# Optimization experiments

Measured on AMD Instinct MI355X. Metric: run time of the kernel, lower is better.

## Reference

```python
import jax, jax.numpy as jnp
import numpy as np
from jax import lax

LIN_DIMS = [(3200, 2048), (2048, 1024), (1024, 512), (512, 256), (256, 128),
            (128, 64), (64, 32), (32, 16), (16, 8), (8, 4), (4, 2), (2, 1)]
BN_EPS = 1e-5


def _conv(x, w, b):
    y = lax.conv_general_dilated(x, w, window_strides=(3, 3),
                                 padding=((1, 1), (1, 1)),
                                 dimension_numbers=('NCHW', 'OIHW', 'NCHW'))
    return y + b.reshape(1, -1, 1, 1)


def _bn(x, g, b):
    # training-mode BatchNorm2d: biased batch statistics over (N, H, W)
    m = jnp.mean(x, axis=(0, 2, 3), keepdims=True)
    v = jnp.var(x, axis=(0, 2, 3), keepdims=True)
    return (x - m) * lax.rsqrt(v + BN_EPS) * g.reshape(1, -1, 1, 1) + b.reshape(1, -1, 1, 1)


def setup_inputs() -> dict:
    key = jax.random.key(0)
    ks = iter(jax.random.split(key, 64))
    d = {}
    d['x'] = jax.random.normal(next(ks), (64, 512, 40, 40), jnp.float32)
    d['conv1_w'] = jax.random.normal(next(ks), (256, 512, 3, 3), jnp.float32) / np.sqrt(512 * 9)
    d['conv1_b'] = jnp.zeros((256,), jnp.float32)
    d['bn1_g'] = jnp.ones((256,), jnp.float32)
    d['bn1_b'] = jnp.zeros((256,), jnp.float32)
    d['conv2_w'] = jax.random.normal(next(ks), (128, 256, 3, 3), jnp.float32) / np.sqrt(256 * 9)
    d['conv2_b'] = jnp.zeros((128,), jnp.float32)
    d['bn2_g'] = jnp.ones((128,), jnp.float32)
    d['bn2_b'] = jnp.zeros((128,), jnp.float32)
    for i, (fin, fout) in enumerate(LIN_DIMS):
        d[f'w{i+3}'] = jax.random.normal(next(ks), (fout, fin), jnp.float32) / np.sqrt(fin)
        d[f'b{i+3}'] = jax.random.normal(next(ks), (fout,), jnp.float32) * 0.01
    return d


def reference(x, conv1_w, conv1_b, bn1_g, bn1_b, conv2_w, conv2_b, bn2_g, bn2_b,
              w3, b3, w4, b4, w5, b5, w6, b6, w7, b7, w8, b8, w9, b9,
              w10, b10, w11, b11, w12, b12, w13, b13, w14, b14):
    h = _bn(_conv(x, conv1_w, conv1_b), bn1_g, bn1_b)          # [B,256,14,14]
    h = _bn(_conv(h, conv2_w, conv2_b), bn2_g, bn2_b)          # [B,128,5,5]
    h = h.reshape(h.shape[0], 3200)
    for w, b in [(w3, b3), (w4, b4), (w5, b5), (w6, b6), (w7, b7), (w8, b8),
                 (w9, b9), (w10, b10), (w11, b11), (w12, b12), (w13, b13), (w14, b14)]:
        h = h @ w.T + b
    return jax.nn.sigmoid(h)                                   # [B,1]
```

## Files before the change

kernel.cpp:

```cpp
#include <hip/hip_runtime.h>
#include <cstdint>
#include <cstddef>

typedef short bf16x8 __attribute__((ext_vector_type(8)));
typedef float f32x4 __attribute__((ext_vector_type(4)));

__device__ __forceinline__ unsigned short f2bf(float f) {
  union { float f; unsigned u; } v; v.f = f;
  unsigned r = v.u + 0x7fffu + ((v.u >> 16) & 1u);
  return (unsigned short)(r >> 16);
}

#define GLOAD_LDS16(gp, lp)                                            \
  __builtin_amdgcn_global_load_lds(                                    \
      (const __attribute__((address_space(1))) void*)(const void*)(gp),\
      (__attribute__((address_space(3))) void*)(void*)(lp), 16, 0, 0)

__global__ __launch_bounds__(256) void cast1(const float* __restrict__ w1,
                                             unsigned short* __restrict__ W1b) {
  int i = blockIdx.x * 256 + threadIdx.x;
  float4 v = ((const float4*)w1)[i];
  ushort4 o;
  o.x = f2bf(v.x); o.y = f2bf(v.y); o.z = f2bf(v.z); o.w = f2bf(v.w);
  ((ushort4*)W1b)[i] = o;
}

__global__ __launch_bounds__(256) void im2col1(const float* __restrict__ x,
                                               unsigned short* __restrict__ A1) {
  __shared__ float buf[64 * 126];
  int t = threadIdx.x;
  int cc = blockIdx.x, oh = blockIdx.y, n = blockIdx.z;
  int ci0 = cc * 64;
  int ih0 = oh * 3 - 1;
  for (int rowid = t; rowid < 192; rowid += 256) {
    int c = rowid / 3, r = rowid - c * 3;
    buf[c * 126 + r * 42 + 0] = 0.f;
    buf[c * 126 + r * 42 + 41] = 0.f;
  }
  for (int idx = t; idx < 1920; idx += 256) {
    int row = idx / 10, ch = idx - row * 10;
    int c = row / 3, r = row - c * 3;
    int ih = ih0 + r;
    float4 v = make_float4(0.f, 0.f, 0.f, 0.f);
    if ((unsigned)ih < 40u)
      v = *(const float4*)(x + (((size_t)n * 512 + ci0 + c) * 40 + ih) * 40 + ch * 4);
    float* dst = buf + c * 126 + r * 42 + 1 + ch * 4;
    dst[0] = v.x; dst[1] = v.y; dst[2] = v.z; dst[3] = v.w;
  }
  __syncthreads();
  for (int idx = t; idx < 2016; idx += 256) {
    int ow = idx / 144, q4 = idx - ow * 144;
    int kk = q4 * 4;
    unsigned short vv[4];
#pragma unroll
    for (int j = 0; j < 4; ++j) {
      int k = kk + j;
      int c = k / 9, rr = k - c * 9;
      int kh = rr / 3, kw = rr - kh * 3;
      vv[j] = f2bf(buf[c * 126 + kh * 42 + 3 * ow + kw]);
    }
    ushort4 o; o.x = vv[0]; o.y = vv[1]; o.z = vv[2]; o.w = vv[3];
    *(ushort4*)(A1 + ((size_t)(n * 196 + oh * 14 + ow)) * 4608 + cc * 576 + kk) = o;
  }
}

template <int BM, int BN>
__global__ __launch_bounds__(256) void gemm_bf16(const unsigned short* __restrict__ A,
                                                 const unsigned short* __restrict__ B,
                                                 float* __restrict__ Cp,
                                                 int M, int N, int K, int k_chunk) {
  __shared__ __align__(16) unsigned short As[BM * 32];
  __shared__ __align__(16) unsigned short Bs[BN * 32];
  constexpr int MT = BM / 32;
  constexpr int NT = BN / 32;
  int m0 = blockIdx.x * BM;
  int n0 = blockIdx.y * BN;
  Cp += (size_t)blockIdx.z * M * N;
  int k_begin = blockIdx.z * k_chunk;
  int t = threadIdx.x;
  int q = (t & 63) >> 4, mr = t & 15;
  int wm = ((t >> 6) & 1) * (BM / 2);
  int wn = (t >> 7) * (BN / 2);
  f32x4 acc[MT][NT] = {};

  for (int k0 = k_begin; k0 < k_begin + k_chunk; k0 += 32) {
    __syncthreads();
#pragma unroll
    for (int i = 0; i < BM / 64; ++i) {
      int c = t + i * 256;
      GLOAD_LDS16(A + (size_t)(m0 + (c >> 2)) * K + k0 + (c & 3) * 8, As + c * 8);
    }
#pragma unroll
    for (int i = 0; i < BN / 64; ++i) {
      int c = t + i * 256;
      GLOAD_LDS16(B + (size_t)(n0 + (c >> 2)) * K + k0 + (c & 3) * 8, Bs + c * 8);
    }
    __syncthreads();
    bf16x8 af[MT], bfr[NT];
#pragma unroll
    for (int s = 0; s < MT; ++s)
      af[s] = *((const bf16x8*)(As + (wm + s * 16 + mr) * 32 + q * 8));
#pragma unroll
    for (int nt = 0; nt < NT; ++nt)
      bfr[nt] = *((const bf16x8*)(Bs + (wn + nt * 16 + mr) * 32 + q * 8));
#pragma unroll
    for (int nt = 0; nt < NT; ++nt)
#pragma unroll
      for (int s = 0; s < MT; ++s)
        acc[s][nt] = __builtin_amdgcn_mfma_f32_16x16x32_bf16(af[s], bfr[nt], acc[s][nt], 0, 0, 0);
  }
#pragma unroll
  for (int s = 0; s < MT; ++s)
#pragma unroll
    for (int nt = 0; nt < NT; ++nt)
#pragma unroll
      for (int r = 0; r < 4; ++r)
        Cp[(size_t)(m0 + wm + s * 16 + q * 4 + r) * N + n0 + wn + nt * 16 + mr] = acc[s][nt][r];
}

__global__ __launch_bounds__(256) void reduce1_scatter(const float* __restrict__ C1P,
                                                       unsigned short* __restrict__ A2,
                                                       float* __restrict__ SUM1,
                                                       float* __restrict__ SQ1) {
  __shared__ __align__(16) unsigned short row[2304];
  int m2 = blockIdx.x, t = threadIdx.x;
  int n = m2 / 25, sp = m2 - n * 25;
  int oh = sp / 5, ow = sp - oh * 5;
  float s = 0.f, s2 = 0.f;
#pragma unroll
  for (int r = 0; r < 9; ++r) {
    int kh = r / 3, kw = r - kh * 3;
    int ih = 3 * oh - 1 + kh, iw = 3 * ow - 1 + kw;
    float v = 0.f;
    if (ih >= 0 && iw >= 0) {
      size_t off = (size_t)(n * 196 + ih * 14 + iw) * 256 + t;
      v = C1P[off] + C1P[3211264 + off];
      s += v; s2 += v * v;
    }
    row[t * 9 + r] = f2bf(v);
  }
  atomicAdd(&SUM1[t], s);
  atomicAdd(&SQ1[t], s2);
  __syncthreads();
  uint4* dst = (uint4*)(A2 + (size_t)m2 * 2304);
  const uint4* src = (const uint4*)row;
  for (int i = t; i < 288; i += 256) dst[i] = src[i];
}

__global__ __launch_bounds__(256) void prep2(const float* __restrict__ w2,
                                             const float* __restrict__ g1,
                                             const float* __restrict__ b1,
                                             const float* __restrict__ SUM1,
                                             const float* __restrict__ SQ1,
                                             unsigned short* __restrict__ W2s,
                                             float* __restrict__ T) {
  int bid = blockIdx.x, t = threadIdx.x;
  if (bid < 1152) {
    int idx = bid * 256 + t;
    int k2 = idx % 2304; int ci = k2 / 9;
    float mean = SUM1[ci] * (1.f / 12544.f);
    float var = SQ1[ci] * (1.f / 12544.f) - mean * mean;
    float sc = g1[ci] * rsqrtf(var + 1e-5f);
    W2s[idx] = f2bf(w2[idx] * sc);
  } else {
    int b2 = bid - 1152;
    int sp = b2 >> 7, n = b2 & 127;
    int oh = sp / 5, ow = sp - oh * 5;
    float p = 0.f;
    for (int k2 = t; k2 < 2304; k2 += 256) {
      int ci = k2 / 9, r = k2 - ci * 9;
      int ih = 3 * oh - 1 + r / 3, iw = 3 * ow - 1 + r % 3;
      if (ih >= 0 && iw >= 0) {
        float mean = SUM1[ci] * (1.f / 12544.f);
        float var = SQ1[ci] * (1.f / 12544.f) - mean * mean;
        float sc = g1[ci] * rsqrtf(var + 1e-5f);
        float sh = b1[ci] - mean * sc;
        p += w2[n * 2304 + k2] * sh;
      }
    }
    __shared__ float red[256];
    red[t] = p; __syncthreads();
    for (int s = 128; s > 0; s >>= 1) {
      if (t < s) red[t] += red[t + s];
      __syncthreads();
    }
    if (t == 0) T[sp * 128 + n] = red[0];
  }
}

__global__ void reduce2_k(const float* __restrict__ C2P, const float* __restrict__ T,
                          float* __restrict__ C2, float* __restrict__ SUM2,
                          float* __restrict__ SQ2) {
  int c = threadIdx.x;
  int r0 = blockIdx.x * 16;
  float s = 0.f, s2 = 0.f;
  for (int r = 0; r < 16; ++r) {
    int m = r0 + r, sp = m % 25;
    size_t off = (size_t)m * 128 + c;
    float v = T[sp * 128 + c];
#pragma unroll
    for (int k = 0; k < 8; ++k) v += C2P[(size_t)k * 204800 + off];
    C2[off] = v;
    s += v; s2 += v * v;
  }
  atomicAdd(&SUM2[c], s);
  atomicAdd(&SQ2[c], s2);
}

__global__ void mlp_head(const float* w14, const float* b14,
                         const float* w13, const float* b13,
                         const float* w12, const float* b12,
                         const float* w11, const float* b11,
                         const float* w10, const float* b10,
                         const float* w9,  const float* b9,
                         const float* w8,  const float* b8,
                         const float* w7,  const float* b7,
                         float* __restrict__ r_out, float* __restrict__ c_out) {
  __shared__ float ra[256], rb[256];
  int t = threadIdx.x;
  float cs = 0.f;
  if (t < 2) ra[t] = w14[t];
  if (t == 0) cs = b14[0];
  __syncthreads();
  const float* Ws[7] = {w13, w12, w11, w10, w9, w8, w7};
  const float* Bs[7] = {b13, b12, b11, b10, b9, b8, b7};
  const int fouts[7] = {2, 4, 8, 16, 32, 64, 128};
  float* cur = ra; float* nxt = rb;
  for (int s = 0; s < 7; ++s) {
    int fo = fouts[s], fi = fo * 2;
    if (t == 0) {
      float d = 0.f;
      for (int i = 0; i < fo; ++i) d += cur[i] * Bs[s][i];
      cs += d;
    }
    if (t < fi) {
      float a = 0.f;
      const float* W = Ws[s];
      for (int i = 0; i < fo; ++i) a += cur[i] * W[i * fi + t];
      nxt[t] = a;
    }
    __syncthreads();
    float* tmp = cur; cur = nxt; nxt = tmp;
  }
  r_out[t] = cur[t];
  if (t == 0) c_out[0] = cs;
}

__global__ void mlp_stage(const float* __restrict__ W, const float* __restrict__ bt,
                          const float* __restrict__ r_in, const float* __restrict__ c_in,
                          float* __restrict__ r_out, float* __restrict__ c_out,
                          int fin, int fout) {
  __shared__ float red[256];
  int t = threadIdx.x;
  int jl = t & 31, ig = t >> 5;
  int j = blockIdx.x * 32 + jl;
  int chunk = fout >> 3;
  int i0 = ig * chunk;
  float acc = 0.f;
  for (int i = i0; i < i0 + chunk; ++i)
    acc += r_in[i] * W[(size_t)i * fin + j];
  red[t] = acc;
  __syncthreads();
  if (ig == 0) {
    float s = 0.f;
#pragma unroll
    for (int u = 0; u < 8; ++u) s += red[u * 32 + jl];
    r_out[j] = s;
  }
  if (blockIdx.x == 0) {
    __syncthreads();
    float p = 0.f;
    for (int i = t; i < fout; i += 256) p += r_in[i] * bt[i];
    red[t] = p;
    __syncthreads();
    for (int s = 128; s > 0; s >>= 1) {
      if (t < s) red[t] += red[t + s];
      __syncthreads();
    }
    if (t == 0) c_out[0] = red[0] + c_in[0];
  }
}

__global__ void final_k(const float* __restrict__ C2, const float* __restrict__ SUM2,
                        const float* __restrict__ SQ2, const float* __restrict__ g2,
                        const float* __restrict__ b2, const float* __restrict__ r,
                        const float* __restrict__ c_in, float* __restrict__ out) {
  int n = blockIdx.x;
  int t = threadIdx.x;
  float acc = 0.f;
  for (int j = t; j < 3200; j += 256) {
    int c = j / 25, sp = j - c * 25;
    float mean = SUM2[c] * (1.f / 1600.f);
    float var = SQ2[c] * (1.f / 1600.f) - mean * mean;
    float sc = g2[c] / sqrtf(var + 1e-5f);
    float sh = b2[c] - mean * sc;
    float v = C2[((size_t)n * 25 + sp) * 128 + c] * sc + sh;
    acc += v * r[j];
  }
  __shared__ float red[256];
  red[t] = acc;
  __syncthreads();
  for (int s = 128; s > 0; s >>= 1) {
    if (t < s) red[t] += red[t + s];
    __syncthreads();
  }
  if (t == 0) {
    float z = red[0] + c_in[0];
    out[n] = 1.f / (1.f + expf(-z));
  }
}

static constexpr size_t OFF_A1   = 0;
static constexpr size_t OFF_C1P  = 115605504;
static constexpr size_t OFF_A2   = 141295616;
static constexpr size_t OFF_C2P  = 148668416;
static constexpr size_t OFF_C2   = 155222016;
static constexpr size_t OFF_W1B  = 156041216;
static constexpr size_t OFF_W2S  = 158400512;
static constexpr size_t OFF_T    = 158990336;
static constexpr size_t OFF_STATS= 159003136;
static constexpr size_t OFF_RA   = 159007232;
static constexpr size_t OFF_RB   = 159020288;
static constexpr size_t OFF_CA   = 159033344;
static constexpr size_t OFF_CB   = 159033472;

extern "C" void kernel_launch(void* const* d_in, const int* in_sizes, int n_in,
                              void* d_out, int out_size, void* d_ws, size_t ws_size,
                              hipStream_t stream) {
  const float* x   = (const float*)d_in[0];
  const float* w1  = (const float*)d_in[1];
  const float* g1  = (const float*)d_in[3];
  const float* bb1 = (const float*)d_in[4];
  const float* w2  = (const float*)d_in[5];
  const float* g2  = (const float*)d_in[7];
  const float* bb2 = (const float*)d_in[8];

  char* ws = (char*)d_ws;
  unsigned short* A1  = (unsigned short*)(ws + OFF_A1);
  float*          C1P = (float*)(ws + OFF_C1P);
  unsigned short* A2  = (unsigned short*)(ws + OFF_A2);
  float*          C2P = (float*)(ws + OFF_C2P);
  float*          C2  = (float*)(ws + OFF_C2);
  unsigned short* W1b = (unsigned short*)(ws + OFF_W1B);
  unsigned short* W2s = (unsigned short*)(ws + OFF_W2S);
  float*          T   = (float*)(ws + OFF_T);
  float* SUM1 = (float*)(ws + OFF_STATS);
  float* SQ1  = (float*)(ws + OFF_STATS + 1024);
  float* SUM2 = (float*)(ws + OFF_STATS + 2048);
  float* SQ2  = (float*)(ws + OFF_STATS + 3072);
  float* RA   = (float*)(ws + OFF_RA);
  float* RB   = (float*)(ws + OFF_RB);
  float* CA   = (float*)(ws + OFF_CA);
  float* CB   = (float*)(ws + OFF_CB);

  hipMemsetAsync(ws + OFF_STATS, 0, 4096, stream);

  cast1<<<1152, 256, 0, stream>>>(w1, W1b);

  im2col1<<<dim3(8, 14, 64), 256, 0, stream>>>(x, A1);
  gemm_bf16<128, 64><<<dim3(98, 4, 2), 256, 0, stream>>>(A1, W1b, C1P, 12544, 256, 4608, 2304);

  reduce1_scatter<<<1600, 256, 0, stream>>>(C1P, A2, SUM1, SQ1);

  prep2<<<4352, 256, 0, stream>>>(w2, g1, bb1, SUM1, SQ1, W2s, T);

  gemm_bf16<64, 64><<<dim3(25, 2, 8), 256, 0, stream>>>(A2, W2s, C2P, 1600, 128, 2304, 288);
  reduce2_k<<<100, 128, 0, stream>>>(C2P, T, C2, SUM2, SQ2);

  mlp_head<<<1, 256, 0, stream>>>(
      (const float*)d_in[31], (const float*)d_in[32],
      (const float*)d_in[29], (const float*)d_in[30],
      (const float*)d_in[27], (const float*)d_in[28],
      (const float*)d_in[25], (const float*)d_in[26],
      (const float*)d_in[23], (const float*)d_in[24],
      (const float*)d_in[21], (const float*)d_in[22],
      (const float*)d_in[19], (const float*)d_in[20],
      (const float*)d_in[17], (const float*)d_in[18],
      RA, CA);
  mlp_stage<<<16, 256, 0, stream>>>((const float*)d_in[15], (const float*)d_in[16],
                                    RA, CA, RB, CB, 512, 256);
  mlp_stage<<<32, 256, 0, stream>>>((const float*)d_in[13], (const float*)d_in[14],
                                    RB, CB, RA, CA, 1024, 512);
  mlp_stage<<<64, 256, 0, stream>>>((const float*)d_in[11], (const float*)d_in[12],
                                    RA, CA, RB, CB, 2048, 1024);
  mlp_stage<<<100, 256, 0, stream>>>((const float*)d_in[9], (const float*)d_in[10],
                                     RB, CB, RA, CA, 3200, 2048);

  final_k<<<64, 256, 0, stream>>>(C2, SUM2, SQ2, g2, bb2, RA, CA, (float*)d_out);
}
```

Before: 867.0 us.

## Replace im2col with implicit-GEMM conv1 fused with BN stats and scatter

Conv1 no longer builds a 115 MB im2col matrix. The input is instead transposed once into a padded NHWC bf16 buffer, and the GEMM gathers its A tiles directly from it as an implicit GEMM with a (kh,kw,ci) K ordering. The GEMM epilogue now accumulates the BN1 sum and sum-of-squares with shuffle reductions plus atomics, and scatters bf16 outputs straight into the conv2 A2 layout. This removes the split-K partial buffer and the separate reduce/scatter kernel. The BN shift-correction table shrinks to four border classes. The trade-offs are no split-K, smaller 64x64 tiles with one barrier pair per 32-wide K step, uncoalesced scattered 2-byte stores, and an extra memset of A2.

```diff
diff --git a/kernel.cpp b/kernel.cpp
--- a/kernel.cpp
+++ b/kernel.cpp
@@ -17,50 +17,166 @@
       (__attribute__((address_space(3))) void*)(void*)(lp), 16, 0, 0)
 
 __global__ __launch_bounds__(256) void cast1(const float* __restrict__ w1,
-                                             unsigned short* __restrict__ W1b) {
-  int i = blockIdx.x * 256 + threadIdx.x;
-  float4 v = ((const float4*)w1)[i];
-  ushort4 o;
-  o.x = f2bf(v.x); o.y = f2bf(v.y); o.z = f2bf(v.z); o.w = f2bf(v.w);
-  ((ushort4*)W1b)[i] = o;
-}
-
-__global__ __launch_bounds__(256) void im2col1(const float* __restrict__ x,
-                                               unsigned short* __restrict__ A1) {
-  __shared__ float buf[64 * 126];
-  int t = threadIdx.x;
-  int cc = blockIdx.x, oh = blockIdx.y, n = blockIdx.z;
-  int ci0 = cc * 64;
-  int ih0 = oh * 3 - 1;
-  for (int rowid = t; rowid < 192; rowid += 256) {
-    int c = rowid / 3, r = rowid - c * 3;
-    buf[c * 126 + r * 42 + 0] = 0.f;
-    buf[c * 126 + r * 42 + 41] = 0.f;
-  }
-  for (int idx = t; idx < 1920; idx += 256) {
-    int row = idx / 10, ch = idx - row * 10;
-    int c = row / 3, r = row - c * 3;
-    int ih = ih0 + r;
-    float4 v = make_float4(0.f, 0.f, 0.f, 0.f);
-    if ((unsigned)ih < 40u)
-      v = *(const float4*)(x + (((size_t)n * 512 + ci0 + c) * 40 + ih) * 40 + ch * 4);
-    float* dst = buf + c * 126 + r * 42 + 1 + ch * 4;
-    dst[0] = v.x; dst[1] = v.y; dst[2] = v.z; dst[3] = v.w;
+                                             unsigned short* __restrict__ W1r) {
+  int idx = blockIdx.x * 256 + threadIdx.x;
+  int co = idx >> 9, ci = idx & 511;
+  const float* src = w1 + (size_t)idx * 9;
+#pragma unroll
+  for (int r = 0; r < 9; ++r)
+    W1r[(size_t)co * 4608 + r * 512 + ci] = f2bf(src[r]);
+}
+
+__global__ __launch_bounds__(256) void transpose_x(const float* __restrict__ x,
+                                                   unsigned short* __restrict__ xT) {
+  __shared__ float lds[64 * 41];
+  int t = threadIdx.x;
+  int cc = blockIdx.x, ihp = blockIdx.y, img = blockIdx.z;
+  int ih = ihp - 1;
+  bool rowvalid = (unsigned)ih < 40u;
+  if (rowvalid) {
+    for (int idx = t; idx < 640; idx += 256) {
+      int row = idx / 10, q = idx - row * 10;
+      float4 v = *(const float4*)(x + (((size_t)img * 512 + cc * 64 + row) * 40 + ih) * 40 + q * 4);
+      float* d = lds + row * 41 + q * 4;
+      d[0] = v.x; d[1] = v.y; d[2] = v.z; d[3] = v.w;
+    }
   }
   __syncthreads();
-  for (int idx = t; idx < 2016; idx += 256) {
-    int ow = idx / 144, q4 = idx - ow * 144;
-    int kk = q4 * 4;
+  for (int idx = t; idx < 672; idx += 256) {
+    int iwp = idx >> 4, u = idx & 15;
+    int iw = iwp - 1;
+    bool ok = rowvalid && (unsigned)iw < 40u;
+    ushort4 o;
     unsigned short vv[4];
 #pragma unroll
-    for (int j = 0; j < 4; ++j) {
-      int k = kk + j;
-      int c = k / 9, rr = k - c * 9;
-      int kh = rr / 3, kw = rr - kh * 3;
-      vv[j] = f2bf(buf[c * 126 + kh * 42 + 3 * ow + kw]);
-    }
-    ushort4 o; o.x = vv[0]; o.y = vv[1]; o.z = vv[2]; o.w = vv[3];
-    *(ushort4*)(A1 + ((size_t)(n * 196 + oh * 14 + ow)) * 4608 + cc * 576 + kk) = o;
+    for (int j = 0; j < 4; ++j)
+      vv[j] = ok ? f2bf(lds[(u * 4 + j) * 41 + iw]) : (unsigned short)0;
+    o.x = vv[0]; o.y = vv[1]; o.z = vv[2]; o.w = vv[3];
+    *(ushort4*)(xT + (((size_t)img * 42 + ihp) * 42 + iwp) * 512 + cc * 64 + u * 4) = o;
+  }
+}
+
+__global__ __launch_bounds__(256) void gemm1_fused(const unsigned short* __restrict__ xT,
+                                                   const unsigned short* __restrict__ W1r,
+                                                   unsigned short* __restrict__ A2,
+                                                   float* __restrict__ SUM1,
+                                                   float* __restrict__ SQ1) {
+  __shared__ __align__(16) unsigned short As[64 * 32];
+  __shared__ __align__(16) unsigned short Bs[64 * 32];
+  int t = threadIdx.x;
+  int m0 = blockIdx.x * 64;
+  int n0 = blockIdx.y * 64;
+  int arow = m0 + (t >> 2);
+  int img_s = arow / 196, sp_s = arow - img_s * 196;
+  int oh_s = sp_s / 14, ow_s = sp_s - oh_s * 14;
+  const unsigned short* Abase =
+      xT + (((size_t)img_s * 42 + 3 * oh_s) * 42 + 3 * ow_s) * 512 + (t & 3) * 8;
+  const unsigned short* Bbase = W1r + (size_t)(n0 + (t >> 2)) * 4608 + (t & 3) * 8;
+  int q = (t & 63) >> 4, mr = t & 15;
+  int wm = ((t >> 6) & 1) * 32;
+  int wn = (t >> 7) * 32;
+  f32x4 acc[2][2] = {};
+
+  for (int kc = 0; kc < 144; ++kc) {
+    int r = kc >> 4;
+    int kh = (r >= 6) ? 2 : (r >= 3 ? 1 : 0);
+    int kw = r - 3 * kh;
+    int aoff = (kh * 42 + kw) * 512 + ((kc & 15) << 5);
+    __syncthreads();
+    GLOAD_LDS16(Abase + aoff, As + t * 8);
+    GLOAD_LDS16(Bbase + kc * 32, Bs + t * 8);
+    __syncthreads();
+    bf16x8 af[2], bfr[2];
+#pragma unroll
+    for (int s = 0; s < 2; ++s)
+      af[s] = *((const bf16x8*)(As + (wm + s * 16 + mr) * 32 + q * 8));
+#pragma unroll
+    for (int nt = 0; nt < 2; ++nt)
+      bfr[nt] = *((const bf16x8*)(Bs + (wn + nt * 16 + mr) * 32 + q * 8));
+#pragma unroll
+    for (int nt = 0; nt < 2; ++nt)
+#pragma unroll
+      for (int s = 0; s < 2; ++s)
+        acc[s][nt] = __builtin_amdgcn_mfma_f32_16x16x32_bf16(af[s], bfr[nt], acc[s][nt], 0, 0, 0);
+  }
+
+#pragma unroll
+  for (int nt = 0; nt < 2; ++nt) {
+    float cs = 0.f, cq = 0.f;
+#pragma unroll
+    for (int s = 0; s < 2; ++s)
+#pragma unroll
+      for (int rr = 0; rr < 4; ++rr) {
+        float v = acc[s][nt][rr];
+        cs += v; cq += v * v;
+      }
+    cs += __shfl_xor(cs, 16, 64); cq += __shfl_xor(cq, 16, 64);
+    cs += __shfl_xor(cs, 32, 64); cq += __shfl_xor(cq, 32, 64);
+    if (q == 0) {
+      int col = n0 + wn + nt * 16 + mr;
+      atomicAdd(&SUM1[col], cs);
+      atomicAdd(&SQ1[col], cq);
+    }
+  }
+
+#pragma unroll
+  for (int s = 0; s < 2; ++s)
+#pragma unroll
+    for (int rr = 0; rr < 4; ++rr) {
+      int m = m0 + wm + s * 16 + q * 4 + rr;
+      int img = m / 196, sp = m - img * 196;
+      int oh1 = sp / 14, ow1 = sp - oh1 * 14;
+      int oh2 = (oh1 + 1) / 3, kh2 = (oh1 + 1) - 3 * oh2;
+      int ow2 = (ow1 + 1) / 3, kw2 = (ow1 + 1) - 3 * ow2;
+      size_t dst = (size_t)(img * 25 + oh2 * 5 + ow2) * 2304 + (kh2 * 3 + kw2) * 256;
+#pragma unroll
+      for (int nt = 0; nt < 2; ++nt)
+        A2[dst + n0 + wn + nt * 16 + mr] = f2bf(acc[s][nt][rr]);
+    }
+}
+
+__global__ __launch_bounds__(256) void prep2(const float* __restrict__ w2,
+                                             const float* __restrict__ g1,
+                                             const float* __restrict__ b1,
+                                             const float* __restrict__ SUM1,
+                                             const float* __restrict__ SQ1,
+                                             unsigned short* __restrict__ W2s,
+                                             float* __restrict__ T4) {
+  int bid = blockIdx.x, t = threadIdx.x;
+  if (bid < 128) {
+    int idx = bid * 256 + t;
+    int co = idx >> 8, ci = idx & 255;
+    float mean = SUM1[ci] * (1.f / 12544.f);
+    float var = SQ1[ci] * (1.f / 12544.f) - mean * mean;
+    float sc = g1[ci] * rsqrtf(var + 1e-5f);
+    const float* src = w2 + (size_t)idx * 9;
+#pragma unroll
+    for (int r = 0; r < 9; ++r)
+      W2s[(size_t)co * 2304 + r * 256 + ci] = f2bf(src[r] * sc);
+  } else {
+    int b2 = bid - 128;
+    int cls = b2 >> 7, co = b2 & 127;
+    int ci = t;
+    float mean = SUM1[ci] * (1.f / 12544.f);
+    float var = SQ1[ci] * (1.f / 12544.f) - mean * mean;
+    float sc = g1[ci] * rsqrtf(var + 1e-5f);
+    float sh = b1[ci] - mean * sc;
+    const float* src = w2 + ((size_t)co * 256 + ci) * 9;
+    float p = 0.f;
+#pragma unroll
+    for (int r = 0; r < 9; ++r) {
+      int kh = r / 3, kw = r - 3 * kh;
+      bool ok = ((cls & 2) || kh > 0) && ((cls & 1) || kw > 0);
+      if (ok) p += src[r];
+    }
+    p *= sh;
+    __shared__ float red[256];
+    red[t] = p; __syncthreads();
+    for (int s = 128; s > 0; s >>= 1) {
+      if (t < s) red[t] += red[t + s];
+      __syncthreads();
+    }
+    if (t == 0) T4[cls * 128 + co] = red[0];
   }
 }
 
@@ -118,77 +234,7 @@
         Cp[(size_t)(m0 + wm + s * 16 + q * 4 + r) * N + n0 + wn + nt * 16 + mr] = acc[s][nt][r];
 }
 
-__global__ __launch_bounds__(256) void reduce1_scatter(const float* __restrict__ C1P,
-                                                       unsigned short* __restrict__ A2,
-                                                       float* __restrict__ SUM1,
-                                                       float* __restrict__ SQ1) {
-  __shared__ __align__(16) unsigned short row[2304];
-  int m2 = blockIdx.x, t = threadIdx.x;
-  int n = m2 / 25, sp = m2 - n * 25;
-  int oh = sp / 5, ow = sp - oh * 5;
-  float s = 0.f, s2 = 0.f;
-#pragma unroll
-  for (int r = 0; r < 9; ++r) {
-    int kh = r / 3, kw = r - kh * 3;
-    int ih = 3 * oh - 1 + kh, iw = 3 * ow - 1 + kw;
-    float v = 0.f;
-    if (ih >= 0 && iw >= 0) {
-      size_t off = (size_t)(n * 196 + ih * 14 + iw) * 256 + t;
-      v = C1P[off] + C1P[3211264 + off];
-      s += v; s2 += v * v;
-    }
-    row[t * 9 + r] = f2bf(v);
-  }
-  atomicAdd(&SUM1[t], s);
-  atomicAdd(&SQ1[t], s2);
-  __syncthreads();
-  uint4* dst = (uint4*)(A2 + (size_t)m2 * 2304);
-  const uint4* src = (const uint4*)row;
-  for (int i = t; i < 288; i += 256) dst[i] = src[i];
-}
-
-__global__ __launch_bounds__(256) void prep2(const float* __restrict__ w2,
-                                             const float* __restrict__ g1,
-                                             const float* __restrict__ b1,
-                                             const float* __restrict__ SUM1,
-                                             const float* __restrict__ SQ1,
-                                             unsigned short* __restrict__ W2s,
-                                             float* __restrict__ T) {
-  int bid = blockIdx.x, t = threadIdx.x;
-  if (bid < 1152) {
-    int idx = bid * 256 + t;
-    int k2 = idx % 2304; int ci = k2 / 9;
-    float mean = SUM1[ci] * (1.f / 12544.f);
-    float var = SQ1[ci] * (1.f / 12544.f) - mean * mean;
-    float sc = g1[ci] * rsqrtf(var + 1e-5f);
-    W2s[idx] = f2bf(w2[idx] * sc);
-  } else {
-    int b2 = bid - 1152;
-    int sp = b2 >> 7, n = b2 & 127;
-    int oh = sp / 5, ow = sp - oh * 5;
-    float p = 0.f;
-    for (int k2 = t; k2 < 2304; k2 += 256) {
-      int ci = k2 / 9, r = k2 - ci * 9;
-      int ih = 3 * oh - 1 + r / 3, iw = 3 * ow - 1 + r % 3;
-      if (ih >= 0 && iw >= 0) {
-        float mean = SUM1[ci] * (1.f / 12544.f);
-        float var = SQ1[ci] * (1.f / 12544.f) - mean * mean;
-        float sc = g1[ci] * rsqrtf(var + 1e-5f);
-        float sh = b1[ci] - mean * sc;
-        p += w2[n * 2304 + k2] * sh;
-      }
-    }
-    __shared__ float red[256];
-    red[t] = p; __syncthreads();
-    for (int s = 128; s > 0; s >>= 1) {
-      if (t < s) red[t] += red[t + s];
-      __syncthreads();
-    }
-    if (t == 0) T[sp * 128 + n] = red[0];
-  }
-}
-
-__global__ void reduce2_k(const float* __restrict__ C2P, const float* __restrict__ T,
+__global__ void reduce2_k(const float* __restrict__ C2P, const float* __restrict__ T4,
                           float* __restrict__ C2, float* __restrict__ SUM2,
                           float* __restrict__ SQ2) {
   int c = threadIdx.x;
@@ -196,8 +242,10 @@
   float s = 0.f, s2 = 0.f;
   for (int r = 0; r < 16; ++r) {
     int m = r0 + r, sp = m % 25;
+    int oh = sp / 5, ow = sp - oh * 5;
+    int cls = ((oh > 0) ? 2 : 0) | ((ow > 0) ? 1 : 0);
     size_t off = (size_t)m * 128 + c;
-    float v = T[sp * 128 + c];
+    float v = T4[cls * 128 + c];
 #pragma unroll
     for (int k = 0; k < 8; ++k) v += C2P[(size_t)k * 204800 + off];
     C2[off] = v;
@@ -310,19 +358,18 @@
   }
 }
 
-static constexpr size_t OFF_A1   = 0;
-static constexpr size_t OFF_C1P  = 115605504;
-static constexpr size_t OFF_A2   = 141295616;
-static constexpr size_t OFF_C2P  = 148668416;
-static constexpr size_t OFF_C2   = 155222016;
-static constexpr size_t OFF_W1B  = 156041216;
-static constexpr size_t OFF_W2S  = 158400512;
-static constexpr size_t OFF_T    = 158990336;
-static constexpr size_t OFF_STATS= 159003136;
-static constexpr size_t OFF_RA   = 159007232;
-static constexpr size_t OFF_RB   = 159020288;
-static constexpr size_t OFF_CA   = 159033344;
-static constexpr size_t OFF_CB   = 159033472;
+static constexpr size_t OFF_XT   = 0;
+static constexpr size_t OFF_A2   = 115605504;
+static constexpr size_t OFF_C2P  = 122978304;
+static constexpr size_t OFF_C2   = 129531904;
+static constexpr size_t OFF_W1R  = 130351104;
+static constexpr size_t OFF_W2S  = 132710400;
+static constexpr size_t OFF_T4   = 133300224;
+static constexpr size_t OFF_STATS= 133302272;
+static constexpr size_t OFF_RA   = 133306368;
+static constexpr size_t OFF_RB   = 133319424;
+static constexpr size_t OFF_CA   = 133332480;
+static constexpr size_t OFF_CB   = 133332608;
 
 extern "C" void kernel_launch(void* const* d_in, const int* in_sizes, int n_in,
                               void* d_out, int out_size, void* d_ws, size_t ws_size,
@@ -336,14 +383,13 @@
   const float* bb2 = (const float*)d_in[8];
 
   char* ws = (char*)d_ws;
-  unsigned short* A1  = (unsigned short*)(ws + OFF_A1);
-  float*          C1P = (float*)(ws + OFF_C1P);
+  unsigned short* xT  = (unsigned short*)(ws + OFF_XT);
   unsigned short* A2  = (unsigned short*)(ws + OFF_A2);
   float*          C2P = (float*)(ws + OFF_C2P);
   float*          C2  = (float*)(ws + OFF_C2);
-  unsigned short* W1b = (unsigned short*)(ws + OFF_W1B);
+  unsigned short* W1r = (unsigned short*)(ws + OFF_W1R);
   unsigned short* W2s = (unsigned short*)(ws + OFF_W2S);
-  float*          T   = (float*)(ws + OFF_T);
+  float*          T4  = (float*)(ws + OFF_T4);
   float* SUM1 = (float*)(ws + OFF_STATS);
   float* SQ1  = (float*)(ws + OFF_STATS + 1024);
   float* SUM2 = (float*)(ws + OFF_STATS + 2048);
@@ -354,18 +400,17 @@
   float* CB   = (float*)(ws + OFF_CB);
 
   hipMemsetAsync(ws + OFF_STATS, 0, 4096, stream);
-
-  cast1<<<1152, 256, 0, stream>>>(w1, W1b);
-
-  im2col1<<<dim3(8, 14, 64), 256, 0, stream>>>(x, A1);
-  gemm_bf16<128, 64><<<dim3(98, 4, 2), 256, 0, stream>>>(A1, W1b, C1P, 12544, 256, 4608, 2304);
-
-  reduce1_scatter<<<1600, 256, 0, stream>>>(C1P, A2, SUM1, SQ1);
-
-  prep2<<<4352, 256, 0, stream>>>(w2, g1, bb1, SUM1, SQ1, W2s, T);
+  hipMemsetAsync(A2, 0, 7372800, stream);
+
+  cast1<<<512, 256, 0, stream>>>(w1, W1r);
+  transpose_x<<<dim3(8, 42, 64), 256, 0, stream>>>(x, xT);
+
+  gemm1_fused<<<dim3(196, 4), 256, 0, stream>>>(xT, W1r, A2, SUM1, SQ1);
+
+  prep2<<<640, 256, 0, stream>>>(w2, g1, bb1, SUM1, SQ1, W2s, T4);
 
   gemm_bf16<64, 64><<<dim3(25, 2, 8), 256, 0, stream>>>(A2, W2s, C2P, 1600, 128, 2304, 288);
-  reduce2_k<<<100, 128, 0, stream>>>(C2P, T, C2, SUM2, SQ2);
+  reduce2_k<<<100, 128, 0, stream>>>(C2P, T4, C2, SUM2, SQ2);
 
   mlp_head<<<1, 256, 0, stream>>>(
       (const float*)d_in[31], (const float*)d_in[32],
```

After: 849.3 us. 2.0% less time.
